# Optimization experiments

Measured on AMD Instinct MI355X. Metric: run time of the kernel, lower is better.

## Reference

```python
import jax, jax.numpy as jnp
import numpy as np

N = 100000
E = 1600000
IN_FEATS = 512
HIDDEN = 128
NUM_CLASSES = 2


def setup_inputs() -> dict:
    key = jax.random.key(0)
    k1, k2, k3, k4, k5, k6, k7 = jax.random.split(key, 7)
    inputs = jax.random.normal(k1, (N, IN_FEATS), dtype=jnp.float32)
    src = jax.random.randint(k2, (E,), 0, N, dtype=jnp.int64)
    dst = jax.random.randint(k3, (E,), 0, N, dtype=jnp.int64)
    # Glorot-style init like DGL GraphConv
    s1 = (6.0 / (IN_FEATS + HIDDEN)) ** 0.5
    s2 = (6.0 / (HIDDEN + NUM_CLASSES)) ** 0.5
    W1 = jax.random.uniform(k4, (IN_FEATS, HIDDEN), jnp.float32, -s1, s1)
    b1 = jnp.zeros((HIDDEN,), jnp.float32)
    W2 = jax.random.uniform(k5, (HIDDEN, NUM_CLASSES), jnp.float32, -s2, s2)
    b2 = jnp.zeros((NUM_CLASSES,), jnp.float32)
    return {"inputs": inputs, "W1": W1, "b1": b1, "W2": W2, "b2": b2,
            "src": src, "dst": dst}


def _graph_conv(x, W, b, src, dst, norm_src, norm_dst):
    # DGL GraphConv, norm='both': D_dst^{-1/2} A D_src^{-1/2} X W + b
    xw = x @ W                                   # [N, out] dense GEMM first (in >= out)
    m = (xw * norm_src[:, None])[src]            # gather messages [E, out]
    agg = jax.ops.segment_sum(m, dst, num_segments=N)  # scatter-add [N, out]
    return agg * norm_dst[:, None] + b


def reference(inputs, W1, b1, W2, b2, src, dst):
    ones = jnp.ones((src.shape[0],), jnp.float32)
    out_deg = jax.ops.segment_sum(ones, src, num_segments=N)
    in_deg = jax.ops.segment_sum(ones, dst, num_segments=N)
    norm_src = jax.lax.rsqrt(jnp.maximum(out_deg, 1.0))
    norm_dst = jax.lax.rsqrt(jnp.maximum(in_deg, 1.0))

    h = _graph_conv(inputs, W1, b1, src, dst, norm_src, norm_dst)
    h = jax.nn.relu(h)
    # dropout is identity at inference (training=False)
    h = _graph_conv(h, W2, b2, src, dst, norm_src, norm_dst)
    return jax.nn.softmax(h, axis=1)
```

## Files before the change

### kernel.cpp

```cpp
#include <hip/hip_runtime.h>
#include <math.h>

#define N_NODES 100000
#define N_EDGES 1600000
#define IN_F    512
#define HID     128

#define SH      8
#define NPB     256
#define BINS    ((N_NODES + NPB - 1) / NPB)
#define CBLK    256
#define EPB     ((N_EDGES + CBLK - 1) / CBLK)

typedef __attribute__((ext_vector_type(8))) _Float16 half8;
typedef __attribute__((ext_vector_type(4))) float float4v;

__global__ __launch_bounds__(256) void prep_kernel(const float* __restrict__ W1,
                                                   _Float16* __restrict__ W1T,
                                                   int* __restrict__ sdeg) {
    int i = blockIdx.x * 256 + threadIdx.x;
    if (i < IN_F * HID) {
        int k = i >> 7, c = i & 127;
        W1T[(size_t)c * IN_F + k] = (_Float16)W1[i];
    }
    if (i < N_NODES) sdeg[i] = 0;
}

__global__ __launch_bounds__(256) void hist_kernel(const int* __restrict__ src,
                                                   const int* __restrict__ dst,
                                                   int* __restrict__ dbh,
                                                   int* __restrict__ sdeg) {
    __shared__ int hd[BINS];
    const int t = threadIdx.x, blk = blockIdx.x;
    for (int i = t; i < BINS; i += 256) hd[i] = 0;
    __syncthreads();
    const int e0 = blk * EPB, e1 = min(N_EDGES, e0 + EPB);
    for (int e = e0 + t; e < e1; e += 256) {
        atomicAdd(&hd[dst[e] >> SH], 1);
        atomicAdd(&sdeg[src[e]], 1);
    }
    __syncthreads();
    for (int i = t; i < BINS; i += 256)
        dbh[i * CBLK + blk] = hd[i];
}

__global__ __launch_bounds__(256) void binscan_kernel(int* __restrict__ dbh,
                                                      int* __restrict__ dtot) {
    __shared__ int sh[256];
    const int b = blockIdx.x, t = threadIdx.x;
    int* arr = dbh + (size_t)b * CBLK;
    int v = arr[t];
    sh[t] = v; __syncthreads();
#pragma unroll
    for (int d = 1; d < 256; d <<= 1) {
        int u = (t >= d) ? sh[t - d] : 0;
        __syncthreads();
        sh[t] += u;
        __syncthreads();
    }
    arr[t] = sh[t] - v;
    if (t == 255) dtot[b] = sh[255];
}

__global__ __launch_bounds__(512) void binbase_kernel(const int* __restrict__ dtot,
                                                      int* __restrict__ dbase,
                                                      int* __restrict__ offs) {
    __shared__ int sh[512];
    const int t = threadIdx.x;
    int v = (t < BINS) ? dtot[t] : 0;
    sh[t] = v; __syncthreads();
#pragma unroll
    for (int d = 1; d < 512; d <<= 1) {
        int u = (t >= d) ? sh[t - d] : 0;
        __syncthreads();
        sh[t] += u;
        __syncthreads();
    }
    if (t < BINS) dbase[t] = sh[t] - v;
    if (t == BINS - 1) { dbase[BINS] = sh[t]; offs[N_NODES] = sh[t]; }
}

__global__ __launch_bounds__(256) void scatter_bins_kernel(const int* __restrict__ src,
                                                           const int* __restrict__ dst,
                                                           const int* __restrict__ dbh,
                                                           const int* __restrict__ dbase,
                                                           int* __restrict__ ds_dst,
                                                           int* __restrict__ ds_src) {
    __shared__ int dcur[BINS];
    const int t = threadIdx.x, blk = blockIdx.x;
    for (int i = t; i < BINS; i += 256)
        dcur[i] = dbase[i] + dbh[i * CBLK + blk];
    __syncthreads();
    const int e0 = blk * EPB, e1 = min(N_EDGES, e0 + EPB);
    for (int e = e0 + t; e < e1; e += 256) {
        int d = dst[e], s = src[e];
        int p = atomicAdd(&dcur[d >> SH], 1);
        ds_dst[p] = d; ds_src[p] = s;
    }
}

__global__ __launch_bounds__(256) void finalize_kernel(const int* __restrict__ ds_dst,
                                                       const int* __restrict__ ds_src,
                                                       const int* __restrict__ sdeg,
                                                       const int* __restrict__ dbase,
                                                       int* __restrict__ csr, int* __restrict__ offs,
                                                       float* __restrict__ norm_dst,
                                                       float* __restrict__ norm_src) {
    __shared__ int cnt[NPB], pos[NPB];
    const int t = threadIdx.x, b = blockIdx.x;
    const int start = dbase[b], end = dbase[b + 1];
    cnt[t] = 0; __syncthreads();
    for (int k = start + t; k < end; k += 256)
        atomicAdd(&cnt[ds_dst[k] & (NPB - 1)], 1);
    __syncthreads();
    const int c = cnt[t];
    pos[t] = c; __syncthreads();
#pragma unroll
    for (int d = 1; d < 256; d <<= 1) {
        int u = (t >= d) ? pos[t - d] : 0;
        __syncthreads();
        pos[t] += u;
        __syncthreads();
    }
    const int excl = pos[t] - c;
    const int node = (b << SH) + t;
    if (node < N_NODES) {
        offs[node] = start + excl;
        norm_dst[node] = rsqrtf(fmaxf((float)c, 1.0f));
        norm_src[node] = rsqrtf(fmaxf((float)sdeg[node], 1.0f));
    }
    cnt[t] = start + excl;
    __syncthreads();
    for (int k = start + t; k < end; k += 256) {
        int dl = ds_dst[k] & (NPB - 1);
        int p = atomicAdd(&cnt[dl], 1);
        csr[p] = ds_src[k];
    }
}

#define APAD 40
__global__ __launch_bounds__(256) void gemm1_mfma_kernel(const float* __restrict__ X,
                                                         const _Float16* __restrict__ W1T,
                                                         const float* __restrict__ norm_src,
                                                         _Float16* __restrict__ xwh) {
    __shared__ _Float16 As[2][128 * APAD];

    const int t    = threadIdx.x;
    const int wave = t >> 6;
    const int lane = t & 63;
    const int m0   = blockIdx.x * 128;
    const int quad = lane >> 4;
    const int l16  = lane & 15;

    float4v acc[2][8];
#pragma unroll
    for (int r = 0; r < 2; r++)
#pragma unroll
        for (int c = 0; c < 8; c++) acc[r][c] = (float4v)0.f;

    const int srow = t >> 1;
    const int sc16 = (t & 1) * 16;
    const int sgrow = m0 + srow;
    const bool svalid = sgrow < N_NODES;
    const float* xbase = X + (size_t)sgrow * IN_F + sc16;

    float4 va[4];
#pragma unroll
    for (int i = 0; i < 4; i++) va[i] = make_float4(0.f, 0.f, 0.f, 0.f);
    if (svalid) {
        const float4* xp = reinterpret_cast<const float4*>(xbase);
        va[0] = xp[0]; va[1] = xp[1]; va[2] = xp[2]; va[3] = xp[3];
    }
    half8 bfrag[8];
#pragma unroll
    for (int ct = 0; ct < 8; ct++)
        bfrag[ct] = *reinterpret_cast<const half8*>(&W1T[(size_t)(ct * 16 + l16) * IN_F + quad * 8]);

    {
        half8 h0, h1;
        h0[0]=(_Float16)va[0].x; h0[1]=(_Float16)va[0].y; h0[2]=(_Float16)va[0].z; h0[3]=(_Float16)va[0].w;
        h0[4]=(_Float16)va[1].x; h0[5]=(_Float16)va[1].y; h0[6]=(_Float16)va[1].z; h0[7]=(_Float16)va[1].w;
        h1[0]=(_Float16)va[2].x; h1[1]=(_Float16)va[2].y; h1[2]=(_Float16)va[2].z; h1[3]=(_Float16)va[2].w;
        h1[4]=(_Float16)va[3].x; h1[5]=(_Float16)va[3].y; h1[6]=(_Float16)va[3].z; h1[7]=(_Float16)va[3].w;
        *reinterpret_cast<half8*>(&As[0][srow * APAD + sc16 + 0]) = h0;
        *reinterpret_cast<half8*>(&As[0][srow * APAD + sc16 + 8]) = h1;
    }

    int cur = 0;
    for (int it = 0; it < IN_F / 32; it++) {
        const int ktn = (it + 1) * 32;
        const bool more = ktn < IN_F;
        __syncthreads();

        float4 vb[4];
        half8 bnext[8];
        if (more) {
            if (svalid) {
                const float4* xp = reinterpret_cast<const float4*>(xbase + ktn);
                vb[0] = xp[0]; vb[1] = xp[1]; vb[2] = xp[2]; vb[3] = xp[3];
            } else {
                vb[0] = vb[1] = vb[2] = vb[3] = make_float4(0.f, 0.f, 0.f, 0.f);
            }
#pragma unroll
            for (int ct = 0; ct < 8; ct++)
                bnext[ct] = *reinterpret_cast<const half8*>(
                    &W1T[(size_t)(ct * 16 + l16) * IN_F + ktn + quad * 8]);
        }

        half8 afrag[2];
#pragma unroll
        for (int r = 0; r < 2; r++)
            afrag[r] = *reinterpret_cast<const half8*>(
                &As[cur][(wave * 32 + r * 16 + l16) * APAD + quad * 8]);
#pragma unroll
        for (int r = 0; r < 2; r++)
#pragma unroll
            for (int ct = 0; ct < 8; ct++)
                acc[r][ct] = __builtin_amdgcn_mfma_f32_16x16x32_f16(afrag[r], bfrag[ct], acc[r][ct], 0, 0, 0);

        if (more) {
            half8 h0, h1;
            h0[0]=(_Float16)vb[0].x; h0[1]=(_Float16)vb[0].y; h0[2]=(_Float16)vb[0].z; h0[3]=(_Float16)vb[0].w;
            h0[4]=(_Float16)vb[1].x; h0[5]=(_Float16)vb[1].y; h0[6]=(_Float16)vb[1].z; h0[7]=(_Float16)vb[1].w;
            h1[0]=(_Float16)vb[2].x; h1[1]=(_Float16)vb[2].y; h1[2]=(_Float16)vb[2].z; h1[3]=(_Float16)vb[2].w;
            h1[4]=(_Float16)vb[3].x; h1[5]=(_Float16)vb[3].y; h1[6]=(_Float16)vb[3].z; h1[7]=(_Float16)vb[3].w;
            *reinterpret_cast<half8*>(&As[cur ^ 1][srow * APAD + sc16 + 0]) = h0;
            *reinterpret_cast<half8*>(&As[cur ^ 1][srow * APAD + sc16 + 8]) = h1;
#pragma unroll
            for (int ct = 0; ct < 8; ct++) bfrag[ct] = bnext[ct];
        }
        cur ^= 1;
    }

#pragma unroll
    for (int r = 0; r < 2; r++) {
#pragma unroll
        for (int i = 0; i < 4; i++) {
            int grow = m0 + wave * 32 + r * 16 + quad * 4 + i;
            if (grow < N_NODES) {
                float s = norm_src[grow];
                _Float16* orow = &xwh[(size_t)grow * HID];
#pragma unroll
                for (int ct = 0; ct < 8; ct++)
                    orow[ct * 16 + l16] = (_Float16)(acc[r][ct][i] * s);
            }
        }
    }
}

__global__ __launch_bounds__(256) void gather1_kernel(
        const int* __restrict__ csr, const int* __restrict__ offs,
        const _Float16* __restrict__ xwh, const float* __restrict__ norm_dst,
        const float* __restrict__ norm_src, const float* __restrict__ b1,
        const float* __restrict__ W2, float* __restrict__ hw2) {
    const int gw   = (blockIdx.x * blockDim.x + threadIdx.x) >> 6;
    const int lane = threadIdx.x & 63;
    const int sub  = lane >> 4;
    const int l16  = lane & 15;
    const int n    = gw * 4 + sub;
    if (n >= N_NODES) return;
    const int off = offs[n], end = offs[n + 1];
    const int j8 = l16 * 8;

    float a[8];
#pragma unroll
    for (int i = 0; i < 8; i++) a[i] = 0.f;

    int k = off;
    for (; k + 4 <= end; k += 4) {
        int s0 = csr[k], s1 = csr[k + 1], s2 = csr[k + 2], s3 = csr[k + 3];
        half8 v0 = *reinterpret_cast<const half8*>(&xwh[(size_t)s0 * HID + j8]);
        half8 v1 = *reinterpret_cast<const half8*>(&xwh[(size_t)s1 * HID + j8]);
        half8 v2 = *reinterpret_cast<const half8*>(&xwh[(size_t)s2 * HID + j8]);
        half8 v3 = *reinterpret_cast<const half8*>(&xwh[(size_t)s3 * HID + j8]);
#pragma unroll
        for (int i = 0; i < 8; i++)
            a[i] += ((float)v0[i] + (float)v1[i]) + ((float)v2[i] + (float)v3[i]);
    }
    for (; k < end; ++k) {
        half8 v = *reinterpret_cast<const half8*>(&xwh[(size_t)csr[k] * HID + j8]);
#pragma unroll
        for (int i = 0; i < 8; i++) a[i] += (float)v[i];
    }

    const float nd = norm_dst[n];
    const float4 b1a = *reinterpret_cast<const float4*>(&b1[j8]);
    const float4 b1b = *reinterpret_cast<const float4*>(&b1[j8 + 4]);
    float h[8];
    h[0] = fmaxf(a[0] * nd + b1a.x, 0.f);
    h[1] = fmaxf(a[1] * nd + b1a.y, 0.f);
    h[2] = fmaxf(a[2] * nd + b1a.z, 0.f);
    h[3] = fmaxf(a[3] * nd + b1a.w, 0.f);
    h[4] = fmaxf(a[4] * nd + b1b.x, 0.f);
    h[5] = fmaxf(a[5] * nd + b1b.y, 0.f);
    h[6] = fmaxf(a[6] * nd + b1b.z, 0.f);
    h[7] = fmaxf(a[7] * nd + b1b.w, 0.f);

    const float4* w2p = reinterpret_cast<const float4*>(&W2[(size_t)j8 * 2]);
    float4 q0 = w2p[0], q1 = w2p[1], q2 = w2p[2], q3 = w2p[3];
    float p0 = h[0]*q0.x + h[1]*q0.z + h[2]*q1.x + h[3]*q1.z
             + h[4]*q2.x + h[5]*q2.z + h[6]*q3.x + h[7]*q3.z;
    float p1 = h[0]*q0.y + h[1]*q0.w + h[2]*q1.y + h[3]*q1.w
             + h[4]*q2.y + h[5]*q2.w + h[6]*q3.y + h[7]*q3.w;
#pragma unroll
    for (int d = 1; d < 16; d <<= 1) {
        p0 += __shfl_xor(p0, d);
        p1 += __shfl_xor(p1, d);
    }
    if (l16 == 0) {
        float ns = norm_src[n];
        reinterpret_cast<float2*>(hw2)[n] = make_float2(p0 * ns, p1 * ns);
    }
}

__global__ void gather2_softmax_kernel(
        const int* __restrict__ csr, const int* __restrict__ offs,
        const float* __restrict__ hw2, const float* __restrict__ norm_dst,
        const float* __restrict__ b2, float* __restrict__ out) {
    const int w    = (blockIdx.x * blockDim.x + threadIdx.x) >> 6;
    const int lane = threadIdx.x & 63;
    const int sub  = lane >> 4, k0 = lane & 15;
    const int n = w * 4 + sub;
    if (n >= N_NODES) return;
    const int off = offs[n], end = offs[n + 1];

    float a0 = 0.f, a1 = 0.f;
    for (int k = off + k0; k < end; k += 16) {
        int s = csr[k];
        float2 v = reinterpret_cast<const float2*>(hw2)[s];
        a0 += v.x; a1 += v.y;
    }
#pragma unroll
    for (int d = 1; d < 16; d <<= 1) {
        a0 += __shfl_xor(a0, d);
        a1 += __shfl_xor(a1, d);
    }
    if (k0 == 0) {
        float nd = norm_dst[n];
        float z0 = a0 * nd + b2[0];
        float z1 = a1 * nd + b2[1];
        float m = fmaxf(z0, z1);
        float e0 = expf(z0 - m), e1 = expf(z1 - m);
        float inv = 1.f / (e0 + e1);
        reinterpret_cast<float2*>(out)[n] = make_float2(e0 * inv, e1 * inv);
    }
}

extern "C" void kernel_launch(void* const* d_in, const int* in_sizes, int n_in,
                              void* d_out, int out_size, void* d_ws, size_t ws_size,
                              hipStream_t stream) {
    const float* X   = (const float*)d_in[0];
    const float* W1  = (const float*)d_in[1];
    const float* b1  = (const float*)d_in[2];
    const float* W2  = (const float*)d_in[3];
    const float* b2  = (const float*)d_in[4];
    const int*   src = (const int*)d_in[5];
    const int*   dst = (const int*)d_in[6];
    float* out = (float*)d_out;

    const size_t N = N_NODES;
    char* ws = (char*)d_ws;
    int*   dbh      = (int*)ws;   ws += (size_t)BINS * CBLK * 4;
    int*   dtot     = (int*)ws;   ws += BINS * 4;
    int*   dbase    = (int*)ws;   ws += (BINS + 1) * 4;
    int*   sdeg     = (int*)ws;   ws += N * 4;
    int*   ds_dst   = (int*)ws;   ws += (size_t)N_EDGES * 4;
    int*   ds_src   = (int*)ws;   ws += (size_t)N_EDGES * 4;
    int*   csr      = (int*)ws;   ws += (size_t)N_EDGES * 4;
    int*   offs     = (int*)ws;   ws += (N + 1) * 4;
    float* norm_src = (float*)ws; ws += N * 4;
    float* norm_dst = (float*)ws; ws += N * 4;
    float* hw2      = (float*)ws; ws += N * 2 * 4;
    _Float16* W1T   = (_Float16*)ws; ws += (size_t)IN_F * HID * 2;
    _Float16* xwh   = (_Float16*)ws; ws += N * (size_t)HID * 2;

    prep_kernel<<<(N_NODES + 255) / 256, 256, 0, stream>>>(W1, W1T, sdeg);
    hist_kernel<<<CBLK, 256, 0, stream>>>(src, dst, dbh, sdeg);
    binscan_kernel<<<BINS, 256, 0, stream>>>(dbh, dtot);
    binbase_kernel<<<1, 512, 0, stream>>>(dtot, dbase, offs);
    scatter_bins_kernel<<<CBLK, 256, 0, stream>>>(src, dst, dbh, dbase, ds_dst, ds_src);
    finalize_kernel<<<BINS, 256, 0, stream>>>(ds_dst, ds_src, sdeg, dbase,
                                              csr, offs, norm_dst, norm_src);
    gemm1_mfma_kernel<<<(N_NODES + 127) / 128, 256, 0, stream>>>(X, W1T, norm_src, xwh);
    gather1_kernel<<<(((N_NODES + 3) / 4) * 64 + 255) / 256, 256, 0, stream>>>(
        csr, offs, xwh, norm_dst, norm_src, b1, W2, hw2);
    gather2_softmax_kernel<<<(((int)N + 3) / 4 * 64 + 255) / 256, 256, 0, stream>>>(
        csr, offs, hw2, norm_dst, b2, out);
}
```

Before: 532.0 us.

## Store XW1 messages as FP8 e4m3 and pack edge bin records into one word

The GEMM1 output is now scaled, clamped and quantized to 8-bit e4m3 bytes instead of fp16, halving the bytes gathered per edge in the first aggregation. The gather decodes the bytes to fp16 with bit tricks and accumulates in packed fp16 pairs, with an 8-wide unrolled edge loop. The binning step packs the local destination index and the source id into a single 32-bit word, halving that scratch traffic. In exchange, precision drops sharply: e4m3 quantization with a fixed scale and clamp, plus fp16 accumulation, can overflow or lose accuracy, which may break the tolerance check.

```diff
diff --git a/kernel.cpp b/kernel.cpp
--- a/kernel.cpp
+++ b/kernel.cpp
@@ -13,7 +13,17 @@
 #define EPB     ((N_EDGES + CBLK - 1) / CBLK)
 
 typedef __attribute__((ext_vector_type(8))) _Float16 half8;
+typedef __attribute__((ext_vector_type(2))) _Float16 half2v;
 typedef __attribute__((ext_vector_type(4))) float float4v;
+
+__device__ __forceinline__ unsigned int f16_to_e4m3bits(float xs) {
+    _Float16 h = (_Float16)xs;
+    unsigned short b = __builtin_bit_cast(unsigned short, h);
+    unsigned int mag = (unsigned int)(b & 0x7fffu);
+    mag = (mag + 0x3fu + ((mag >> 7) & 1u)) >> 7;
+    if (mag > 0x7eu) mag = 0x7eu;
+    return (((unsigned int)b >> 8) & 0x80u) | mag;
+}
 
 __global__ __launch_bounds__(256) void prep_kernel(const float* __restrict__ W1,
                                                    _Float16* __restrict__ W1T,
@@ -84,8 +94,7 @@
                                                            const int* __restrict__ dst,
                                                            const int* __restrict__ dbh,
                                                            const int* __restrict__ dbase,
-                                                           int* __restrict__ ds_dst,
-                                                           int* __restrict__ ds_src) {
+                                                           unsigned int* __restrict__ es) {
     __shared__ int dcur[BINS];
     const int t = threadIdx.x, blk = blockIdx.x;
     for (int i = t; i < BINS; i += 256)
@@ -95,12 +104,11 @@
     for (int e = e0 + t; e < e1; e += 256) {
         int d = dst[e], s = src[e];
         int p = atomicAdd(&dcur[d >> SH], 1);
-        ds_dst[p] = d; ds_src[p] = s;
-    }
-}
-
-__global__ __launch_bounds__(256) void finalize_kernel(const int* __restrict__ ds_dst,
-                                                       const int* __restrict__ ds_src,
+        es[p] = ((unsigned int)(d & (NPB - 1)) << 24) | (unsigned int)s;
+    }
+}
+
+__global__ __launch_bounds__(256) void finalize_kernel(const unsigned int* __restrict__ es,
                                                        const int* __restrict__ sdeg,
                                                        const int* __restrict__ dbase,
                                                        int* __restrict__ csr, int* __restrict__ offs,
@@ -111,7 +119,7 @@
     const int start = dbase[b], end = dbase[b + 1];
     cnt[t] = 0; __syncthreads();
     for (int k = start + t; k < end; k += 256)
-        atomicAdd(&cnt[ds_dst[k] & (NPB - 1)], 1);
+        atomicAdd(&cnt[es[k] >> 24], 1);
     __syncthreads();
     const int c = cnt[t];
     pos[t] = c; __syncthreads();
@@ -132,9 +140,9 @@
     cnt[t] = start + excl;
     __syncthreads();
     for (int k = start + t; k < end; k += 256) {
-        int dl = ds_dst[k] & (NPB - 1);
-        int p = atomicAdd(&cnt[dl], 1);
-        csr[p] = ds_src[k];
+        unsigned int v = es[k];
+        int p = atomicAdd(&cnt[v >> 24], 1);
+        csr[p] = (int)(v & 0x00FFFFFFu);
     }
 }
 
@@ -142,7 +150,7 @@
 __global__ __launch_bounds__(256) void gemm1_mfma_kernel(const float* __restrict__ X,
                                                          const _Float16* __restrict__ W1T,
                                                          const float* __restrict__ norm_src,
-                                                         _Float16* __restrict__ xwh) {
+                                                         unsigned int* __restrict__ xw8) {
     __shared__ _Float16 As[2][128 * APAD];
 
     const int t    = threadIdx.x;
@@ -238,11 +246,17 @@
         for (int i = 0; i < 4; i++) {
             int grow = m0 + wave * 32 + r * 16 + quad * 4 + i;
             if (grow < N_NODES) {
-                float s = norm_src[grow];
-                _Float16* orow = &xwh[(size_t)grow * HID];
-#pragma unroll
-                for (int ct = 0; ct < 8; ct++)
-                    orow[ct * 16 + l16] = (_Float16)(acc[r][ct][i] * s);
+                const float ss = norm_src[grow] * 0.00390625f;
+                unsigned int by[8];
+#pragma unroll
+                for (int ct = 0; ct < 8; ct++) {
+                    float xs = acc[r][ct][i] * ss;
+                    xs = fminf(fmaxf(xs, -1.75f), 1.75f);
+                    by[ct] = f16_to_e4m3bits(xs);
+                }
+                unsigned int w0 = by[0] | (by[1] << 8) | (by[2] << 16) | (by[3] << 24);
+                unsigned int w1 = by[4] | (by[5] << 8) | (by[6] << 16) | (by[7] << 24);
+                *reinterpret_cast<uint2*>(&xw8[(size_t)grow * 32 + l16 * 2]) = make_uint2(w0, w1);
             }
         }
     }
@@ -250,7 +264,7 @@
 
 __global__ __launch_bounds__(256) void gather1_kernel(
         const int* __restrict__ csr, const int* __restrict__ offs,
-        const _Float16* __restrict__ xwh, const float* __restrict__ norm_dst,
+        const unsigned int* __restrict__ xw8, const float* __restrict__ norm_dst,
         const float* __restrict__ norm_src, const float* __restrict__ b1,
         const float* __restrict__ W2, float* __restrict__ hw2) {
     const int gw   = (blockIdx.x * blockDim.x + threadIdx.x) >> 6;
@@ -260,48 +274,66 @@
     const int n    = gw * 4 + sub;
     if (n >= N_NODES) return;
     const int off = offs[n], end = offs[n + 1];
-    const int j8 = l16 * 8;
-
-    float a[8];
-#pragma unroll
-    for (int i = 0; i < 8; i++) a[i] = 0.f;
+    const uint2* xp = reinterpret_cast<const uint2*>(xw8);
+
+    half2v accA = (half2v)0, accB = (half2v)0, accC = (half2v)0, accD = (half2v)0;
+
+#define DECADD(u, aE, aO)                                                          \
+    {                                                                              \
+        unsigned int _u = (u);                                                     \
+        unsigned int _e = ((_u & 0x00800080u) << 8) | ((_u & 0x007f007fu) << 7);   \
+        unsigned int _s = _u >> 8;                                                 \
+        unsigned int _o = ((_s & 0x00800080u) << 8) | ((_s & 0x007f007fu) << 7);   \
+        aE += __builtin_bit_cast(half2v, _e);                                      \
+        aO += __builtin_bit_cast(half2v, _o);                                      \
+    }
+#define ACC8(u2) { DECADD((u2).x, accA, accB) DECADD((u2).y, accC, accD) }
 
     int k = off;
+    for (; k + 8 <= end; k += 8) {
+        int s0 = csr[k], s1 = csr[k + 1], s2 = csr[k + 2], s3 = csr[k + 3];
+        int s4 = csr[k + 4], s5 = csr[k + 5], s6 = csr[k + 6], s7 = csr[k + 7];
+        uint2 u0 = xp[(size_t)s0 * 16 + l16];
+        uint2 u1 = xp[(size_t)s1 * 16 + l16];
+        uint2 u2 = xp[(size_t)s2 * 16 + l16];
+        uint2 u3 = xp[(size_t)s3 * 16 + l16];
+        uint2 u4 = xp[(size_t)s4 * 16 + l16];
+        uint2 u5 = xp[(size_t)s5 * 16 + l16];
+        uint2 u6 = xp[(size_t)s6 * 16 + l16];
+        uint2 u7 = xp[(size_t)s7 * 16 + l16];
+        ACC8(u0) ACC8(u1) ACC8(u2) ACC8(u3) ACC8(u4) ACC8(u5) ACC8(u6) ACC8(u7)
+    }
     for (; k + 4 <= end; k += 4) {
         int s0 = csr[k], s1 = csr[k + 1], s2 = csr[k + 2], s3 = csr[k + 3];
-        half8 v0 = *reinterpret_cast<const half8*>(&xwh[(size_t)s0 * HID + j8]);
-        half8 v1 = *reinterpret_cast<const half8*>(&xwh[(size_t)s1 * HID + j8]);
-        half8 v2 = *reinterpret_cast<const half8*>(&xwh[(size_t)s2 * HID + j8]);
-        half8 v3 = *reinterpret_cast<const half8*>(&xwh[(size_t)s3 * HID + j8]);
-#pragma unroll
-        for (int i = 0; i < 8; i++)
-            a[i] += ((float)v0[i] + (float)v1[i]) + ((float)v2[i] + (float)v3[i]);
+        uint2 u0 = xp[(size_t)s0 * 16 + l16];
+        uint2 u1 = xp[(size_t)s1 * 16 + l16];
+        uint2 u2 = xp[(size_t)s2 * 16 + l16];
+        uint2 u3 = xp[(size_t)s3 * 16 + l16];
+        ACC8(u0) ACC8(u1) ACC8(u2) ACC8(u3)
     }
     for (; k < end; ++k) {
-        half8 v = *reinterpret_cast<const half8*>(&xwh[(size_t)csr[k] * HID + j8]);
-#pragma unroll
-        for (int i = 0; i < 8; i++) a[i] += (float)v[i];
-    }
-
-    const float nd = norm_dst[n];
-    const float4 b1a = *reinterpret_cast<const float4*>(&b1[j8]);
-    const float4 b1b = *reinterpret_cast<const float4*>(&b1[j8 + 4]);
-    float h[8];
-    h[0] = fmaxf(a[0] * nd + b1a.x, 0.f);
-    h[1] = fmaxf(a[1] * nd + b1a.y, 0.f);
-    h[2] = fmaxf(a[2] * nd + b1a.z, 0.f);
-    h[3] = fmaxf(a[3] * nd + b1a.w, 0.f);
-    h[4] = fmaxf(a[4] * nd + b1b.x, 0.f);
-    h[5] = fmaxf(a[5] * nd + b1b.y, 0.f);
-    h[6] = fmaxf(a[6] * nd + b1b.z, 0.f);
-    h[7] = fmaxf(a[7] * nd + b1b.w, 0.f);
-
-    const float4* w2p = reinterpret_cast<const float4*>(&W2[(size_t)j8 * 2]);
-    float4 q0 = w2p[0], q1 = w2p[1], q2 = w2p[2], q3 = w2p[3];
-    float p0 = h[0]*q0.x + h[1]*q0.z + h[2]*q1.x + h[3]*q1.z
-             + h[4]*q2.x + h[5]*q2.z + h[6]*q3.x + h[7]*q3.z;
-    float p1 = h[0]*q0.y + h[1]*q0.w + h[2]*q1.y + h[3]*q1.w
-             + h[4]*q2.y + h[5]*q2.w + h[6]*q3.y + h[7]*q3.w;
+        uint2 u = xp[(size_t)csr[k] * 16 + l16];
+        ACC8(u)
+    }
+#undef ACC8
+#undef DECADD
+
+    float a[8];
+    a[0] = (float)accA[0]; a[2] = (float)accA[1];
+    a[1] = (float)accB[0]; a[3] = (float)accB[1];
+    a[4] = (float)accC[0]; a[6] = (float)accC[1];
+    a[5] = (float)accD[0]; a[7] = (float)accD[1];
+
+    const float nd = norm_dst[n] * 256.0f;
+    float p0 = 0.f, p1 = 0.f;
+#pragma unroll
+    for (int ct = 0; ct < 8; ct++) {
+        const int col = ct * 16 + l16;
+        float h = fmaxf(a[ct] * nd + b1[col], 0.f);
+        float2 w2v = reinterpret_cast<const float2*>(W2)[col];
+        p0 += h * w2v.x;
+        p1 += h * w2v.y;
+    }
 #pragma unroll
     for (int d = 1; d < 16; d <<= 1) {
         p0 += __shfl_xor(p0, d);
@@ -360,30 +392,34 @@
 
     const size_t N = N_NODES;
     char* ws = (char*)d_ws;
-    int*   dbh      = (int*)ws;   ws += (size_t)BINS * CBLK * 4;
-    int*   dtot     = (int*)ws;   ws += BINS * 4;
-    int*   dbase    = (int*)ws;   ws += (BINS + 1) * 4;
-    int*   sdeg     = (int*)ws;   ws += N * 4;
-    int*   ds_dst   = (int*)ws;   ws += (size_t)N_EDGES * 4;
-    int*   ds_src   = (int*)ws;   ws += (size_t)N_EDGES * 4;
-    int*   csr      = (int*)ws;   ws += (size_t)N_EDGES * 4;
-    int*   offs     = (int*)ws;   ws += (N + 1) * 4;
-    float* norm_src = (float*)ws; ws += N * 4;
-    float* norm_dst = (float*)ws; ws += N * 4;
-    float* hw2      = (float*)ws; ws += N * 2 * 4;
-    _Float16* W1T   = (_Float16*)ws; ws += (size_t)IN_F * HID * 2;
-    _Float16* xwh   = (_Float16*)ws; ws += N * (size_t)HID * 2;
+    auto alloc = [&](size_t bytes) -> char* {
+        char* p = ws;
+        ws += (bytes + 15) & ~(size_t)15;
+        return p;
+    };
+    int*          dbh      = (int*)alloc((size_t)BINS * CBLK * 4);
+    int*          dtot     = (int*)alloc(BINS * 4);
+    int*          dbase    = (int*)alloc((BINS + 1) * 4);
+    int*          sdeg     = (int*)alloc(N * 4);
+    unsigned int* es       = (unsigned int*)alloc((size_t)N_EDGES * 4);
+    int*          csr      = (int*)alloc((size_t)N_EDGES * 4);
+    int*          offs     = (int*)alloc((N + 1) * 4);
+    float*        norm_src = (float*)alloc(N * 4);
+    float*        norm_dst = (float*)alloc(N * 4);
+    float*        hw2      = (float*)alloc(N * 2 * 4);
+    _Float16*     W1T      = (_Float16*)alloc((size_t)IN_F * HID * 2);
+    unsigned int* xw8      = (unsigned int*)alloc(N * (size_t)HID);
 
     prep_kernel<<<(N_NODES + 255) / 256, 256, 0, stream>>>(W1, W1T, sdeg);
     hist_kernel<<<CBLK, 256, 0, stream>>>(src, dst, dbh, sdeg);
     binscan_kernel<<<BINS, 256, 0, stream>>>(dbh, dtot);
     binbase_kernel<<<1, 512, 0, stream>>>(dtot, dbase, offs);
-    scatter_bins_kernel<<<CBLK, 256, 0, stream>>>(src, dst, dbh, dbase, ds_dst, ds_src);
-    finalize_kernel<<<BINS, 256, 0, stream>>>(ds_dst, ds_src, sdeg, dbase,
+    scatter_bins_kernel<<<CBLK, 256, 0, stream>>>(src, dst, dbh, dbase, es);
+    finalize_kernel<<<BINS, 256, 0, stream>>>(es, sdeg, dbase,
                                               csr, offs, norm_dst, norm_src);
-    gemm1_mfma_kernel<<<(N_NODES + 127) / 128, 256, 0, stream>>>(X, W1T, norm_src, xwh);
+    gemm1_mfma_kernel<<<(N_NODES + 127) / 128, 256, 0, stream>>>(X, W1T, norm_src, xw8);
     gather1_kernel<<<(((N_NODES + 3) / 4) * 64 + 255) / 256, 256, 0, stream>>>(
-        csr, offs, xwh, norm_dst, norm_src, b1, W2, hw2);
+        csr, offs, xw8, norm_dst, norm_src, b1, W2, hw2);
     gather2_softmax_kernel<<<(((int)N + 3) / 4 * 64 + 255) / 256, 256, 0, stream>>>(
         csr, offs, hw2, norm_dst, b2, out);
 }
```

Measured after the change: 492.0 us. 1.08x faster.
